# Kernel tuning notes

Hardware: AMD Instinct MI355X
Metric: run time of the kernel (lower is better)

## Reference

```python
import jax, jax.numpy as jnp
import numpy as np
import math

B, L, D, H, DEPTH = 2, 1024, 1024, 16, 4
INNER = int(D * 4 * 2 / 3)  # 2730
HD = D // H
SCALE = D ** 0.5


def _get_slopes(n):
    def pow2(n):
        start = 2 ** (-2 ** (-(math.log2(n) - 3)))
        return [start * start ** i for i in range(n)]
    if math.log2(n).is_integer():
        return pow2(n)
    c = 2 ** math.floor(math.log2(n))
    return pow2(c) + _get_slopes(2 * c)[0::2][: n - c]


def setup_inputs() -> dict:
    key = jax.random.key(0)
    ks = jax.random.split(key, 8)
    def rn(k, shape, s=0.02):
        return jax.random.normal(k, shape, dtype=jnp.float32) * s
    return {
        "x": jax.random.normal(ks[0], (B, L, D), dtype=jnp.float32),
        "slopes": jnp.asarray(np.asarray(_get_slopes(H), dtype=np.float32).reshape(H, 1, 1)),
        "gamma_attn": jnp.ones((DEPTH, D), jnp.float32),
        "in_proj_w": rn(ks[1], (DEPTH, 3 * D, D)),
        "in_proj_b": jnp.zeros((DEPTH, 3 * D), jnp.float32),
        "out_proj_w": rn(ks[2], (DEPTH, D, D)),
        "out_proj_b": jnp.zeros((DEPTH, D), jnp.float32),
        "gamma_ff": jnp.ones((DEPTH, D), jnp.float32),
        "ff_w1": rn(ks[3], (DEPTH, 2 * INNER, D)),
        "ff_b1": jnp.zeros((DEPTH, 2 * INNER), jnp.float32),
        "ff_w2": rn(ks[4], (DEPTH, D, INNER)),
        "ff_b2": jnp.zeros((DEPTH, D), jnp.float32),
        "final_gamma": jnp.ones((D,), jnp.float32),
    }


def _rmsnorm(t, gamma):
    # F.normalize(x, dim=-1) * sqrt(dim) * gamma
    n = jnp.linalg.norm(t, axis=-1, keepdims=True)
    return t / jnp.maximum(n, 1e-12) * SCALE * gamma


def reference(x, slopes, gamma_attn, in_proj_w, in_proj_b, out_proj_w, out_proj_b,
              gamma_ff, ff_w1, ff_b1, ff_w2, ff_b2, final_gamma):
    Bsz, Ls, Dm = x.shape
    pos = jnp.arange(Ls)
    # ALiBi bias: -(|i-j|) * per-head slope -> (H, L, L); shared across batch
    alibi = (-jnp.abs(pos[None, :] - pos[:, None]).astype(jnp.float32))[None] * slopes
    for i in range(DEPTH):
        # attention block
        a_in = _rmsnorm(x, gamma_attn[i])
        qkv = a_in @ in_proj_w[i].T + in_proj_b[i]  # (B, L, 3D)
        q, k, v = jnp.split(qkv, 3, axis=-1)
        q = q.reshape(Bsz, Ls, H, HD).transpose(0, 2, 1, 3)
        k = k.reshape(Bsz, Ls, H, HD).transpose(0, 2, 1, 3)
        v = v.reshape(Bsz, Ls, H, HD).transpose(0, 2, 1, 3)
        scores = jnp.einsum('bhqd,bhkd->bhqk', q, k) / math.sqrt(HD) + alibi[None]
        attn = jax.nn.softmax(scores, axis=-1)
        o = jnp.einsum('bhqk,bhkd->bhqd', attn, v).transpose(0, 2, 1, 3).reshape(Bsz, Ls, Dm)
        x = o @ out_proj_w[i].T + out_proj_b[i] + x
        # GEGLU feed-forward block
        f_in = _rmsnorm(x, gamma_ff[i])
        h = f_in @ ff_w1[i].T + ff_b1[i]
        a, gate = jnp.split(h, 2, axis=-1)
        x = (jax.nn.gelu(gate, approximate=False) * a) @ ff_w2[i].T + ff_b2[i] + x
    return _rmsnorm(x, final_gamma)
```

## Files before the change

kernel.cpp:

```cpp
#include <hip/hip_runtime.h>

#define DEPTH   4
#define BSZ     2
#define LSEQ    1024
#define DMODEL  1024
#define NHEAD   16
#define HDIM    64
#define MROWS   (BSZ*LSEQ)
#define INNER   2730
#define INNERP  2752
#define N1      (2*INNER)
#define N1P     (2*INNERP)
#define LOG2E   1.4426950408889634f
#define NSPLIT  2

typedef __bf16 bf16;
typedef bf16  bf16x8 __attribute__((ext_vector_type(8)));
typedef float f32x4  __attribute__((ext_vector_type(4)));
typedef uint32_t u32x4 __attribute__((ext_vector_type(4)));

__device__ inline f32x4 mfma16(bf16x8 a, bf16x8 b, f32x4 c) {
  return __builtin_amdgcn_mfma_f32_16x16x32_bf16(a, b, c, 0, 0, 0);
}

__device__ inline void gload_lds16(const void* g, void* l) {
  __builtin_amdgcn_global_load_lds(
      (const __attribute__((address_space(1))) void*)g,
      (__attribute__((address_space(3))) void*)l, 16, 0, 0);
}

__global__ void conv_bf16_kernel(const float* __restrict__ src, bf16* __restrict__ dst, size_t n) {
  size_t i = ((size_t)blockIdx.x * 256 + threadIdx.x) * 8;
  if (i >= n) return;
  float4 v0 = *(const float4*)(src + i);
  float4 v1 = *(const float4*)(src + i + 4);
  bf16x8 o = { (bf16)v0.x,(bf16)v0.y,(bf16)v0.z,(bf16)v0.w,
               (bf16)v1.x,(bf16)v1.y,(bf16)v1.z,(bf16)v1.w };
  *(bf16x8*)(dst + i) = o;
}

__global__ void conv_w1_kernel(const float* __restrict__ src, bf16* __restrict__ dst) {
  size_t i = ((size_t)blockIdx.x * 256 + threadIdx.x) * 8;
  const size_t tot = (size_t)DEPTH * N1P * DMODEL;
  if (i >= tot) return;
  int d  = (int)(i / ((size_t)N1P * DMODEL));
  int rem = (int)(i % ((size_t)N1P * DMODEL));
  int rp = rem / DMODEL, k = rem % DMODEL;
  int p2 = rp >> 4, w = rp & 15;
  int col = ((p2 >> 1) << 4) + w;
  bf16x8 o;
  if (col >= INNER) {
    o = (bf16x8)(bf16)0.f;
  } else {
    int rs = (p2 & 1) ? (INNER + col) : col;
    const float* s = src + ((size_t)d * N1 + rs) * DMODEL + k;
    float4 v0 = *(const float4*)s;
    float4 v1 = *(const float4*)(s + 4);
    o = bf16x8{ (bf16)v0.x,(bf16)v0.y,(bf16)v0.z,(bf16)v0.w,
                (bf16)v1.x,(bf16)v1.y,(bf16)v1.z,(bf16)v1.w };
  }
  *(bf16x8*)(dst + i) = o;
}

__global__ void conv_b1_kernel(const float* __restrict__ src, float* __restrict__ dst) {
  int i = blockIdx.x * 256 + threadIdx.x;
  if (i >= DEPTH * N1P) return;
  int d = i / N1P, rp = i % N1P;
  int p2 = rp >> 4, w = rp & 15;
  int col = ((p2 >> 1) << 4) + w;
  float v = 0.f;
  if (col < INNER) v = src[d * N1 + ((p2 & 1) ? (INNER + col) : col)];
  dst[i] = v;
}

__global__ void conv_w2_kernel(const float* __restrict__ src, bf16* __restrict__ dst) {
  size_t i = ((size_t)blockIdx.x * 256 + threadIdx.x) * 8;
  const size_t tot = (size_t)DEPTH * DMODEL * INNERP;
  if (i >= tot) return;
  size_t dn = i / INNERP;
  int kp = (int)(i % INNERP);
  const float* s = src + dn * INNER;
  bf16x8 o;
  #pragma unroll
  for (int j = 0; j < 8; ++j) {
    int k = kp + j;
    o[j] = (k < INNER) ? (bf16)s[k] : (bf16)0.f;
  }
  *(bf16x8*)(dst + i) = o;
}

template<bool OUT_BF16>
__global__ __launch_bounds__(256) void rmsnorm_kernel(const float* __restrict__ x,
    const float* __restrict__ gamma, void* __restrict__ out) {
  const int row = blockIdx.x;
  const int tid = threadIdx.x;
  const float4 v = *(const float4*)(x + (size_t)row * DMODEL + tid * 4);
  float ss = v.x*v.x + v.y*v.y + v.z*v.z + v.w*v.w;
  for (int m = 1; m < 64; m <<= 1) ss += __shfl_xor(ss, m);
  __shared__ float ws4[4];
  if ((tid & 63) == 0) ws4[tid >> 6] = ss;
  __syncthreads();
  float tot = ws4[0] + ws4[1] + ws4[2] + ws4[3];
  float scale = 32.0f / fmaxf(sqrtf(tot), 1e-12f);
  const float4 g = *(const float4*)(gamma + tid * 4);
  float o0 = v.x*scale*g.x, o1 = v.y*scale*g.y, o2 = v.z*scale*g.z, o3 = v.w*scale*g.w;
  size_t p = (size_t)row * DMODEL + tid * 4;
  if (OUT_BF16) {
    bf16* ob = (bf16*)out;
    ob[p+0] = (bf16)o0; ob[p+1] = (bf16)o1; ob[p+2] = (bf16)o2; ob[p+3] = (bf16)o3;
  } else {
    *(float4*)((float*)out + p) = make_float4(o0, o1, o2, o3);
  }
}

template<int TN, int EPI, bool CHUNK_M>
__global__ __launch_bounds__(256) void gemm_bt(const bf16* __restrict__ A,
    const bf16* __restrict__ Bw, const float* __restrict__ bias,
    const float* __restrict__ res, void* __restrict__ Cout,
    int M_, int N_, int K_) {
  constexpr int NFR = TN / 32;
  constexpr int BCH = TN / 32;
  __shared__ __attribute__((aligned(16))) bf16 As[2][128 * 64];
  __shared__ __attribute__((aligned(16))) bf16 Bs[2][TN * 64];
  const int tid  = threadIdx.x;
  const int lane = tid & 63;
  const int wid  = tid >> 6;
  const int wr = wid >> 1, wc = wid & 1;

  const int gx = gridDim.x, gy = gridDim.y;
  const int nwg = gx * gy;
  int bid = blockIdx.y * gx + blockIdx.x;
  int swz = bid;
  if ((nwg & 7) == 0) swz = (bid & 7) * (nwg >> 3) + (bid >> 3);
  int mIdx, nIdx;
  if (CHUNK_M) { nIdx = swz % gx; mIdx = swz / gx; }
  else         { mIdx = swz % gy; nIdx = swz / gy; }
  const int m0 = mIdx * 128;
  const int n0 = nIdx * TN;

  const int q = lane & 15, G = lane >> 4;
  const int s7 = q & 7;
  const int srow = tid >> 3;
  const int scol = ((tid & 7) ^ (srow & 7)) << 3;

  f32x4 acc[4][NFR] = {};
  const int nk = K_ >> 6;

  auto stage = [&](int buf, int kt) {
    const int k0 = kt << 6;
    #pragma unroll
    for (int j = 0; j < 4; ++j) {
      gload_lds16(A + (size_t)(m0 + j*32 + srow) * K_ + k0 + scol,
                  &As[buf][(j * 256 + wid * 64) << 3]);
    }
    #pragma unroll
    for (int j = 0; j < BCH; ++j) {
      gload_lds16(Bw + (size_t)(n0 + j*32 + srow) * K_ + k0 + scol,
                  &Bs[buf][(j * 256 + wid * 64) << 3]);
    }
  };

  stage(0, 0);
  asm volatile("s_waitcnt vmcnt(0)" ::: "memory");
  __syncthreads();

  int cur = 0;
  for (int kt = 0; kt < nk; ++kt) {
    if (kt + 1 < nk) stage(cur ^ 1, kt + 1);
    #pragma unroll
    for (int kk = 0; kk < 2; ++kk) {
      const int c0 = kk * 4 + G;
      bf16x8 af[4], bfr[NFR];
      #pragma unroll
      for (int m = 0; m < 4; ++m)
        af[m] = *(const bf16x8*)(&As[cur][(wr*64 + m*16 + q) * 64 + ((c0 ^ s7) << 3)]);
      #pragma unroll
      for (int n = 0; n < NFR; ++n)
        bfr[n] = *(const bf16x8*)(&Bs[cur][(wc*(TN/2) + n*16 + q) * 64 + ((c0 ^ s7) << 3)]);
      #pragma unroll
      for (int m = 0; m < 4; ++m)
        #pragma unroll
        for (int n = 0; n < NFR; ++n)
          acc[m][n] = mfma16(af[m], bfr[n], acc[m][n]);
    }
    asm volatile("s_waitcnt vmcnt(0)" ::: "memory");
    __syncthreads();
    cur ^= 1;
  }

  const int rb = G << 2;
  const int cl = q;
  if (EPI == 2) {
    #pragma unroll
    for (int m = 0; m < 4; ++m) {
      #pragma unroll
      for (int np = 0; np < NFR/2; ++np) {
        int ca = n0 + wc*(TN/2) + (2*np)*16 + cl;
        int cg = ca + 16;
        float ba = bias[ca], bg = bias[cg];
        int colo = ((ca >> 5) << 4) + cl;
        #pragma unroll
        for (int r = 0; r < 4; ++r) {
          int row = m0 + wr*64 + m*16 + rb + r;
          float av = acc[m][2*np][r] + ba;
          float gv = acc[m][2*np+1][r] + bg;
          float gl = 0.5f * gv * (1.f + erff(gv * 0.70710678118654752f));
          ((bf16*)Cout)[(size_t)row * (N_ >> 1) + colo] = (bf16)(av * gl);
        }
      }
    }
  } else {
    #pragma unroll
    for (int m = 0; m < 4; ++m) {
      #pragma unroll
      for (int n = 0; n < NFR; ++n) {
        int col = n0 + wc*(TN/2) + n*16 + cl;
        float bv = bias[col];
        #pragma unroll
        for (int r = 0; r < 4; ++r) {
          int row = m0 + wr*64 + m*16 + rb + r;
          float v = acc[m][n][r] + bv;
          size_t p = (size_t)row * N_ + col;
          if (EPI == 1) ((float*)Cout)[p] = v + res[p];
          else          ((bf16*)Cout)[p] = (bf16)v;
        }
      }
    }
  }
}

__global__ __launch_bounds__(256) void attn_kernel(const bf16* __restrict__ qkv,
    const float* __restrict__ slopes, float* __restrict__ Opart, float* __restrict__ ml) {
  const int tid = threadIdx.x, lane = tid & 63, wid = tid >> 6;
  const int bh = blockIdx.y;
  const int b = bh >> 4, h = bh & 15;
  const int kvz = blockIdx.z;
  const int kv0 = kvz * (LSEQ / NSPLIT);
  const float slope2 = slopes[h] * LOG2E;
  const float SC = 0.125f * LOG2E;
  const int qw = blockIdx.x * 64 + wid * 16;

  __shared__ __attribute__((aligned(16))) bf16     Kt[64 * 72];
  __shared__ __attribute__((aligned(16))) uint32_t V32[64 * 36];
  __shared__ __attribute__((aligned(16))) uint32_t Pl32[4][16 * 36];

  const size_t rs = 3 * DMODEL;
  const size_t base = (size_t)b * LSEQ * rs;

  bf16x8 qf[2];
  {
    const bf16* p = qkv + base + (size_t)(qw + (lane & 15)) * rs + h * HDIM + ((lane >> 4) << 3);
    qf[0] = *(const bf16x8*)p;
    qf[1] = *(const bf16x8*)(p + 32);
  }

  f32x4 accO[4] = {};
  float mrow[4], lrow[4];
  #pragma unroll
  for (int r = 0; r < 4; ++r) { mrow[r] = -1e30f; lrow[r] = 0.f; }

  const int trow = tid >> 2;
  const int tcol = (tid & 3) << 4;

  bf16x8 kreg0, kreg1, vreg0, vreg1;
  {
    const bf16* kp = qkv + base + (size_t)(kv0 + trow) * rs + DMODEL + h * HDIM + tcol;
    kreg0 = *(const bf16x8*)kp; kreg1 = *(const bf16x8*)(kp + 8);
    const bf16* vp = qkv + base + (size_t)(kv0 + trow) * rs + 2 * DMODEL + h * HDIM + tcol;
    vreg0 = *(const bf16x8*)vp; vreg1 = *(const bf16x8*)(vp + 8);
  }

  uint32_t* P32w = &Pl32[wid][0];
  const int q = lane & 15, G = lane >> 4;

  for (int kv = kv0; kv < kv0 + LSEQ / NSPLIT; kv += 64) {
    __syncthreads();
    *(bf16x8*)(Kt + trow * 72 + tcol)     = kreg0;
    *(bf16x8*)(Kt + trow * 72 + tcol + 8) = kreg1;
    {
      u32x4 va = __builtin_bit_cast(u32x4, vreg0);
      u32x4 vb = __builtin_bit_cast(u32x4, vreg1);
      u32x4 pa, pb;
      #pragma unroll
      for (int i = 0; i < 4; ++i) {
        pa[i] = (uint32_t)__shfl_xor((int)va[i], 4);
        pb[i] = (uint32_t)__shfl_xor((int)vb[i], 4);
      }
      const bool oddk = (trow & 1);
      const int d0 = tcol + (oddk ? 8 : 0);
      u32x4 m = oddk ? vb : va;
      u32x4 oo = oddk ? pb : pa;
      const int kpair = trow >> 1;
      const int swz = kpair ^ ((d0 >> 3) << 1);
      #pragma unroll
      for (int i = 0; i < 4; ++i) {
        uint32_t lo = oddk ? oo[i] : m[i];
        uint32_t hi = oddk ? m[i] : oo[i];
        uint32_t w0 = (lo & 0xffffu) | (hi << 16);
        uint32_t w1 = (lo >> 16) | (hi & 0xffff0000u);
        V32[(d0 + 2*i)     * 36 + swz] = w0;
        V32[(d0 + 2*i + 1) * 36 + swz] = w1;
      }
    }
    __syncthreads();

    if (kv + 64 < kv0 + LSEQ / NSPLIT) {
      const bf16* kp = qkv + base + (size_t)(kv + 64 + trow) * rs + DMODEL + h * HDIM + tcol;
      kreg0 = *(const bf16x8*)kp; kreg1 = *(const bf16x8*)(kp + 8);
      const bf16* vp = qkv + base + (size_t)(kv + 64 + trow) * rs + 2 * DMODEL + h * HDIM + tcol;
      vreg0 = *(const bf16x8*)vp; vreg1 = *(const bf16x8*)(vp + 8);
    }

    f32x4 sacc[4] = {};
    __builtin_amdgcn_s_setprio(1);
    #pragma unroll
    for (int nt = 0; nt < 4; ++nt) {
      const bf16* kb = Kt + (nt * 16 + q) * 72 + (G << 3);
      sacc[nt] = mfma16(qf[0], *(const bf16x8*)kb, sacc[nt]);
      sacc[nt] = mfma16(qf[1], *(const bf16x8*)(kb + 32), sacc[nt]);
    }
    __builtin_amdgcn_s_setprio(0);

    float pv[4][4];
    #pragma unroll
    for (int r = 0; r < 4; ++r) {
      int qi = qw + (G << 2) + r;
      float vmax = -1e30f;
      #pragma unroll
      for (int nt = 0; nt < 4; ++nt) {
        int kj = kv + nt * 16 + q;
        float s = sacc[nt][r] * SC - slope2 * fabsf((float)(qi - kj));
        pv[nt][r] = s;
        vmax = fmaxf(vmax, s);
      }
      for (int m = 1; m < 16; m <<= 1) vmax = fmaxf(vmax, __shfl_xor(vmax, m));
      float newmax = fmaxf(mrow[r], vmax);
      float ef = exp2f(mrow[r] - newmax);
      float rsum = 0.f;
      #pragma unroll
      for (int nt = 0; nt < 4; ++nt) {
        float p = exp2f(pv[nt][r] - newmax);
        pv[nt][r] = p;
        rsum += p;
      }
      for (int m = 1; m < 16; m <<= 1) rsum += __shfl_xor(rsum, m);
      lrow[r] = lrow[r] * ef + rsum;
      mrow[r] = newmax;
      #pragma unroll
      for (int dn = 0; dn < 4; ++dn) accO[dn][r] *= ef;
    }

    #pragma unroll
    for (int nt = 0; nt < 4; ++nt) {
      #pragma unroll
      for (int r = 0; r < 4; ++r) {
        float other = __shfl_xor(pv[nt][r], 1);
        if (!(lane & 1)) {
          uint32_t w;
          asm("v_cvt_pk_bf16_f32 %0, %1, %2" : "=v"(w) : "v"(pv[nt][r]), "v"(other));
          int prow = (G << 2) + r;
          int col2 = nt * 8 + (q >> 1);
          P32w[prow * 36 + (col2 ^ ((prow & 7) << 1))] = w;
        }
      }
    }
    asm volatile("s_waitcnt lgkmcnt(0)" ::: "memory");

    __builtin_amdgcn_s_setprio(1);
    #pragma unroll
    for (int chunk = 0; chunk < 2; ++chunk) {
      u32x4 praw = *(const u32x4*)(P32w + q * 36 + chunk * 16 + 4 * (G ^ ((q >> 1) & 3)));
      if (q & 1) praw = __builtin_shufflevector(praw, praw, 2, 3, 0, 1);
      bf16x8 pf = __builtin_bit_cast(bf16x8, praw);
      #pragma unroll
      for (int dn = 0; dn < 4; ++dn) {
        const int d = dn * 16 + q;
        u32x4 raw = *(const u32x4*)(V32 + d * 36 + chunk * 16 + 4 * (G ^ dn));
        if ((lane >> 3) & 1) raw = __builtin_shufflevector(raw, raw, 2, 3, 0, 1);
        bf16x8 vf = __builtin_bit_cast(bf16x8, raw);
        accO[dn] = mfma16(pf, vf, accO[dn]);
      }
    }
    __builtin_amdgcn_s_setprio(0);
  }

  #pragma unroll
  for (int r = 0; r < 4; ++r) {
    int qr = qw + (G << 2) + r;
    size_t obase = ((size_t)(kvz * 32 + bh) * LSEQ + qr) * HDIM;
    #pragma unroll
    for (int dn = 0; dn < 4; ++dn)
      Opart[obase + dn * 16 + q] = accO[dn][r];
    if (q == 0) {
      size_t mb = ((size_t)(kvz * 32 + bh) * LSEQ + qr) * 2;
      ml[mb]     = mrow[r];
      ml[mb + 1] = lrow[r];
    }
  }
}

__global__ __launch_bounds__(256) void attn_combine(const float* __restrict__ Opart,
    const float* __restrict__ ml, bf16* __restrict__ o) {
  int idx = blockIdx.x * 256 + threadIdx.x;
  int bh = idx >> 14;
  int rem = idx & 16383;
  int qr = rem >> 4;
  int d4 = (rem & 15) << 2;
  float mz[NSPLIT], lz[NSPLIT];
  float m = -1e30f;
  #pragma unroll
  for (int z = 0; z < NSPLIT; ++z) {
    size_t rz = ((size_t)(z * 32 + bh) * LSEQ + qr) * 2;
    mz[z] = ml[rz]; lz[z] = ml[rz + 1];
    m = fmaxf(m, mz[z]);
  }
  float wz[NSPLIT];
  float l = 0.f;
  #pragma unroll
  for (int z = 0; z < NSPLIT; ++z) { wz[z] = exp2f(mz[z] - m); l += lz[z] * wz[z]; }
  float inv = 1.f / l;
  float ax = 0, ay = 0, az = 0, aw = 0;
  #pragma unroll
  for (int z = 0; z < NSPLIT; ++z) {
    size_t rz = (size_t)(z * 32 + bh) * LSEQ + qr;
    float4 ov = *(const float4*)(Opart + rz * HDIM + d4);
    ax += ov.x * wz[z]; ay += ov.y * wz[z]; az += ov.z * wz[z]; aw += ov.w * wz[z];
  }
  int b = bh >> 4, h = bh & 15;
  bf16* op = o + ((size_t)(b * LSEQ + qr) * DMODEL + h * HDIM + d4);
  op[0] = (bf16)(ax * inv);
  op[1] = (bf16)(ay * inv);
  op[2] = (bf16)(az * inv);
  op[3] = (bf16)(aw * inv);
}

extern "C" void kernel_launch(void* const* d_in, const int* in_sizes, int n_in,
                              void* d_out, int out_size, void* d_ws, size_t ws_size,
                              hipStream_t stream) {
  const float* x_in      = (const float*)d_in[0];
  const float* slopes    = (const float*)d_in[1];
  const float* g_attn    = (const float*)d_in[2];
  const float* w_in      = (const float*)d_in[3];
  const float* b_in      = (const float*)d_in[4];
  const float* w_out     = (const float*)d_in[5];
  const float* b_out     = (const float*)d_in[6];
  const float* g_ff      = (const float*)d_in[7];
  const float* w1        = (const float*)d_in[8];
  const float* b1        = (const float*)d_in[9];
  const float* w2        = (const float*)d_in[10];
  const float* b2        = (const float*)d_in[11];
  const float* g_final   = (const float*)d_in[12];

  char* p = (char*)d_ws;
  float* xw   = (float*)p;              p += (size_t)MROWS * DMODEL * 4;
  bf16* abuf  = (bf16*)p;               p += (size_t)MROWS * DMODEL * 2;
  bf16* qkvb  = (bf16*)p;               p += (size_t)MROWS * 3 * DMODEL * 2;
  bf16* obuf  = (bf16*)p;               p += (size_t)MROWS * DMODEL * 2;
  bf16* gbuf  = (bf16*)p;               p += (size_t)MROWS * INNERP * 2;
  float* Opart = (float*)p;             p += (size_t)NSPLIT * 32 * LSEQ * HDIM * 4;
  float* mlb   = (float*)p;             p += (size_t)NSPLIT * 32 * LSEQ * 2 * 4;
  bf16* w_in_b  = (bf16*)p;             p += (size_t)DEPTH * 3 * DMODEL * DMODEL * 2;
  bf16* w_out_b = (bf16*)p;             p += (size_t)DEPTH * DMODEL * DMODEL * 2;
  bf16* w1p     = (bf16*)p;             p += (size_t)DEPTH * N1P * DMODEL * 2;
  bf16* w2p     = (bf16*)p;             p += (size_t)DEPTH * DMODEL * INNERP * 2;
  float* b1p    = (float*)p;            p += (size_t)DEPTH * N1P * 4;

  hipMemcpyAsync(xw, x_in, (size_t)MROWS * DMODEL * 4, hipMemcpyDeviceToDevice, stream);

  conv_bf16_kernel<<<6144, 256, 0, stream>>>(w_in, w_in_b, (size_t)DEPTH * 3 * DMODEL * DMODEL);
  conv_bf16_kernel<<<2048, 256, 0, stream>>>(w_out, w_out_b, (size_t)DEPTH * DMODEL * DMODEL);
  conv_w1_kernel<<<11008, 256, 0, stream>>>(w1, w1p);
  conv_b1_kernel<<<86, 256, 0, stream>>>(b1, b1p);
  conv_w2_kernel<<<5504, 256, 0, stream>>>(w2, w2p);

  for (int i = 0; i < DEPTH; ++i) {
    rmsnorm_kernel<true><<<MROWS, 256, 0, stream>>>(xw, g_attn + i * DMODEL, abuf);
    gemm_bt<64, 0, false><<<dim3(48, 16), 256, 0, stream>>>(
        abuf, w_in_b + (size_t)i * 3 * DMODEL * DMODEL, b_in + i * 3 * DMODEL,
        nullptr, qkvb, MROWS, 3 * DMODEL, DMODEL);
    attn_kernel<<<dim3(16, 32, NSPLIT), 256, 0, stream>>>(qkvb, slopes, Opart, mlb);
    attn_combine<<<2048, 256, 0, stream>>>(Opart, mlb, obuf);
    gemm_bt<64, 1, true><<<dim3(16, 16), 256, 0, stream>>>(
        obuf, w_out_b + (size_t)i * DMODEL * DMODEL, b_out + i * DMODEL,
        xw, xw, MROWS, DMODEL, DMODEL);
    rmsnorm_kernel<true><<<MROWS, 256, 0, stream>>>(xw, g_ff + i * DMODEL, abuf);
    gemm_bt<128, 2, false><<<dim3(43, 16), 256, 0, stream>>>(
        abuf, w1p + (size_t)i * N1P * DMODEL, b1p + i * N1P,
        nullptr, gbuf, MROWS, N1P, DMODEL);
    gemm_bt<64, 1, true><<<dim3(16, 16), 256, 0, stream>>>(
        gbuf, w2p + (size_t)i * DMODEL * INNERP, b2 + i * DMODEL,
        xw, xw, MROWS, DMODEL, INNERP);
  }
  rmsnorm_kernel<false><<<MROWS, 256, 0, stream>>>(xw, g_final, d_out);
}
```

Measured before the change: 846.7 us.

## Split-K the residual GEMMs with atomic accumulation and shrink FF1 tile width

The out-projection and FF2 GEMMs now split the K dimension across two z-slices. Each slice atomically adds its partial sum into the fp32 residual buffer, with the bias added only by the first slice. This doubles the workgroup count for these 256-block launches, giving better CU occupancy on a 256-CU part. The FF1 GEMM also moves from 128-wide to 64-wide N tiles to get more workgroups. The cost is atomic traffic, nondeterministic summation order, and less data reuse per tile.

After: 794.5 us. -6.2%, faster.

```diff
diff --git a/kernel.cpp b/kernel.cpp
--- a/kernel.cpp
+++ b/kernel.cpp
@@ -116,8 +116,7 @@
 template<int TN, int EPI, bool CHUNK_M>
 __global__ __launch_bounds__(256) void gemm_bt(const bf16* __restrict__ A,
     const bf16* __restrict__ Bw, const float* __restrict__ bias,
-    const float* __restrict__ res, void* __restrict__ Cout,
-    int M_, int N_, int K_) {
+    void* __restrict__ Cout, int M_, int N_, int Kstr, int nk0, int nkTot) {
   constexpr int NFR = TN / 32;
   constexpr int BCH = TN / 32;
   __shared__ __attribute__((aligned(16))) bf16 As[2][128 * 64];
@@ -126,6 +125,10 @@
   const int lane = tid & 63;
   const int wid  = tid >> 6;
   const int wr = wid >> 1, wc = wid & 1;
+
+  const int z = blockIdx.z;
+  const int nk  = z ? (nkTot - nk0) : nk0;
+  const int kOff = z * (nk0 << 6);
 
   const int gx = gridDim.x, gy = gridDim.y;
   const int nwg = gx * gy;
@@ -144,18 +147,17 @@
   const int scol = ((tid & 7) ^ (srow & 7)) << 3;
 
   f32x4 acc[4][NFR] = {};
-  const int nk = K_ >> 6;
 
   auto stage = [&](int buf, int kt) {
-    const int k0 = kt << 6;
+    const int k0 = kOff + (kt << 6);
     #pragma unroll
     for (int j = 0; j < 4; ++j) {
-      gload_lds16(A + (size_t)(m0 + j*32 + srow) * K_ + k0 + scol,
+      gload_lds16(A + (size_t)(m0 + j*32 + srow) * Kstr + k0 + scol,
                   &As[buf][(j * 256 + wid * 64) << 3]);
     }
     #pragma unroll
     for (int j = 0; j < BCH; ++j) {
-      gload_lds16(Bw + (size_t)(n0 + j*32 + srow) * K_ + k0 + scol,
+      gload_lds16(Bw + (size_t)(n0 + j*32 + srow) * Kstr + k0 + scol,
                   &Bs[buf][(j * 256 + wid * 64) << 3]);
     }
   };
@@ -209,6 +211,20 @@
         }
       }
     }
+  } else if (EPI == 3) {
+    #pragma unroll
+    for (int m = 0; m < 4; ++m) {
+      #pragma unroll
+      for (int n = 0; n < NFR; ++n) {
+        int col = n0 + wc*(TN/2) + n*16 + cl;
+        float bv = (z == 0) ? bias[col] : 0.f;
+        #pragma unroll
+        for (int r = 0; r < 4; ++r) {
+          int row = m0 + wr*64 + m*16 + rb + r;
+          atomicAdd((float*)Cout + (size_t)row * N_ + col, acc[m][n][r] + bv);
+        }
+      }
+    }
   } else {
     #pragma unroll
     for (int m = 0; m < 4; ++m) {
@@ -219,10 +235,7 @@
         #pragma unroll
         for (int r = 0; r < 4; ++r) {
           int row = m0 + wr*64 + m*16 + rb + r;
-          float v = acc[m][n][r] + bv;
-          size_t p = (size_t)row * N_ + col;
-          if (EPI == 1) ((float*)Cout)[p] = v + res[p];
-          else          ((bf16*)Cout)[p] = (bf16)v;
+          ((bf16*)Cout)[(size_t)row * N_ + col] = (bf16)(acc[m][n][r] + bv);
         }
       }
     }
@@ -477,19 +490,19 @@
     rmsnorm_kernel<true><<<MROWS, 256, 0, stream>>>(xw, g_attn + i * DMODEL, abuf);
     gemm_bt<64, 0, false><<<dim3(48, 16), 256, 0, stream>>>(
         abuf, w_in_b + (size_t)i * 3 * DMODEL * DMODEL, b_in + i * 3 * DMODEL,
-        nullptr, qkvb, MROWS, 3 * DMODEL, DMODEL);
+        qkvb, MROWS, 3 * DMODEL, DMODEL, 16, 16);
     attn_kernel<<<dim3(16, 32, NSPLIT), 256, 0, stream>>>(qkvb, slopes, Opart, mlb);
     attn_combine<<<2048, 256, 0, stream>>>(Opart, mlb, obuf);
-    gemm_bt<64, 1, true><<<dim3(16, 16), 256, 0, stream>>>(
+    gemm_bt<64, 3, true><<<dim3(16, 16, 2), 256, 0, stream>>>(
         obuf, w_out_b + (size_t)i * DMODEL * DMODEL, b_out + i * DMODEL,
-        xw, xw, MROWS, DMODEL, DMODEL);
+        xw, MROWS, DMODEL, DMODEL, 8, 16);
     rmsnorm_kernel<true><<<MROWS, 256, 0, stream>>>(xw, g_ff + i * DMODEL, abuf);
-    gemm_bt<128, 2, false><<<dim3(43, 16), 256, 0, stream>>>(
+    gemm_bt<64, 2, false><<<dim3(86, 16), 256, 0, stream>>>(
         abuf, w1p + (size_t)i * N1P * DMODEL, b1p + i * N1P,
-        nullptr, gbuf, MROWS, N1P, DMODEL);
-    gemm_bt<64, 1, true><<<dim3(16, 16), 256, 0, stream>>>(
+        gbuf, MROWS, N1P, DMODEL, 16, 16);
+    gemm_bt<64, 3, true><<<dim3(16, 16, 2), 256, 0, stream>>>(
         gbuf, w2p + (size_t)i * DMODEL * INNERP, b2 + i * DMODEL,
-        xw, xw, MROWS, DMODEL, INNERP);
+        xw, MROWS, DMODEL, INNERP, 22, 43);
   }
   rmsnorm_kernel<false><<<MROWS, 256, 0, stream>>>(xw, g_final, d_out);
 }
```
